# Kernel tuning notes

Measured on AMD Instinct MI355X. Metric: run time of the kernel, lower is better.

## Reference

```python
import jax, jax.numpy as jnp
import numpy as np

N_NODES = 50000
N_EDGES = 800000
IN_DIM, HID_DIM, OUT_DIM = 1024, 256, 512


def setup_inputs() -> dict:
    key = jax.random.key(0)
    ks = jax.random.split(key, 8)
    x = jax.random.normal(ks[0], (N_NODES, IN_DIM), dtype=jnp.float32)
    edge_index = jax.random.randint(ks[1], (2, N_EDGES), 0, N_NODES, dtype=jnp.int64)
    # Glorot-ish scaled weights; PyG SAGEConv: out = lin_l(mean_aggr) + lin_r(x), bias in lin_l
    w1_l = jax.random.normal(ks[2], (HID_DIM, IN_DIM), dtype=jnp.float32) / np.sqrt(IN_DIM)
    w1_r = jax.random.normal(ks[3], (HID_DIM, IN_DIM), dtype=jnp.float32) / np.sqrt(IN_DIM)
    b1 = jnp.zeros((HID_DIM,), dtype=jnp.float32)
    w2_l = jax.random.normal(ks[4], (OUT_DIM, HID_DIM), dtype=jnp.float32) / np.sqrt(HID_DIM)
    w2_r = jax.random.normal(ks[5], (OUT_DIM, HID_DIM), dtype=jnp.float32) / np.sqrt(HID_DIM)
    b2 = jnp.zeros((OUT_DIM,), dtype=jnp.float32)
    return {"x": x, "edge_index": edge_index, "w1_l": w1_l, "w1_r": w1_r, "b1": b1,
            "w2_l": w2_l, "w2_r": w2_r, "b2": b2}


def _sage_conv(x, edge_index, w_l, w_r, b):
    """PyG SAGEConv with mean aggregation: lin_l(mean_{j in N(i)} x_j) + lin_r(x_i)."""
    src, dst = edge_index[0], edge_index[1]
    n = x.shape[0]
    # gather source features and scatter-mean into destinations (the memory-bound part)
    agg = jax.ops.segment_sum(x[src], dst, num_segments=n)          # [N, d_in]
    cnt = jax.ops.segment_sum(jnp.ones_like(src, dtype=x.dtype), dst, num_segments=n)
    mean = agg / jnp.maximum(cnt, 1.0)[:, None]                     # empty neighborhoods -> 0
    return mean @ w_l.T + x @ w_r.T + b


def reference(x, edge_index, w1_l, w1_r, b1, w2_l, w2_r, b2):
    # layer 1 + relu (dropout is identity in eval mode)
    h = jax.nn.relu(_sage_conv(x, edge_index, w1_l, w1_r, b1))
    # final layer, no activation
    return _sage_conv(h, edge_index, w2_l, w2_r, b2)
```

## Files before the change

### kernel.cpp

```cpp
#include <hip/hip_runtime.h>


#define IN_DIM  1024
#define HID_DIM 256
#define OUT_N   512

typedef __attribute__((ext_vector_type(8))) short bf16x8;
typedef __attribute__((ext_vector_type(4))) float f32x4;

static __device__ __forceinline__ unsigned short f2bf(float f) {
  unsigned int u = __float_as_uint(f);
  u += 0x7fffu + ((u >> 16) & 1u);
  return (unsigned short)(u >> 16);
}
static __device__ __forceinline__ float bf2f(unsigned short b) {
  return __uint_as_float(((unsigned int)b) << 16);
}

static __device__ __forceinline__ int load_idx(const void* ei, long long pos, int is64) {
  if (is64) return (int)((const long long*)ei)[pos];
  return ((const int*)ei)[pos];
}

__global__ void k_misc(const unsigned int* __restrict__ ei, int* __restrict__ flag,
                       const float* __restrict__ w1l, const float* __restrict__ w1r,
                       unsigned short* __restrict__ W1c,
                       const float* __restrict__ w2l, const float* __restrict__ w2r,
                       unsigned short* __restrict__ W2c) {
  int b = blockIdx.x;
  if (b == 0) {
    if (threadIdx.x < 64) {
      unsigned int v = ei[2 * threadIdx.x + 1];
      unsigned long long m = __ballot(v == 0u);
      if (threadIdx.x == 0) *flag = (m == ~0ull) ? 1 : 0;
    }
    return;
  }
  b -= 1;
  if (b < 512) {
    int i = b * 256 + threadIdx.x;
    int base = i * 4;
    int n = base / IN_DIM, k = base % IN_DIM;
    const float* s = (n < HID_DIM) ? &w1l[(size_t)n * IN_DIM + k]
                                   : &w1r[(size_t)(n - HID_DIM) * IN_DIM + k];
    float4 v = *(const float4*)s;
    ushort4 o = { f2bf(v.x), f2bf(v.y), f2bf(v.z), f2bf(v.w) };
    *(ushort4*)&W1c[base] = o;
  } else {
    int i = (b - 512) * 256 + threadIdx.x;
    int base = i * 4;
    int n = base >> 9, k = base & 511;
    const float* s = (k < HID_DIM) ? &w2l[(size_t)n * HID_DIM + k]
                                   : &w2r[(size_t)n * HID_DIM + (k - HID_DIM)];
    float4 v = *(const float4*)s;
    ushort4 o = { f2bf(v.x), f2bf(v.y), f2bf(v.z), f2bf(v.w) };
    *(ushort4*)&W2c[base] = o;
  }
}

__global__ void k_cvt_x(const float* __restrict__ x, unsigned short* __restrict__ xbf, int n4) {
  int i = blockIdx.x * 256 + threadIdx.x;
  if (i >= n4) return;
  float4 v = ((const float4*)x)[i];
  ushort4 o = { f2bf(v.x), f2bf(v.y), f2bf(v.z), f2bf(v.w) };
  ((ushort4*)xbf)[i] = o;
}

__global__ void k_deg(const void* ei, int nE, const int* flag, int* deg) {
  int e = blockIdx.x * 256 + threadIdx.x;
  if (e >= nE) return;
  int d = load_idx(ei, (long long)nE + e, *flag);
  atomicAdd(&deg[d], 1);
}

__global__ __launch_bounds__(1024) void k_scan(const int* __restrict__ deg,
                                               int* __restrict__ off, int n) {
  __shared__ int sums[1024];
  int t = threadIdx.x;
  int chunk = (n + 1023) >> 10;
  int base = t * chunk;
  int s = 0;
  for (int i = 0; i < chunk; ++i) { int idx = base + i; if (idx < n) s += deg[idx]; }
  sums[t] = s;
  __syncthreads();
  for (int d = 1; d < 1024; d <<= 1) {
    int v = 0;
    if (t >= d) v = sums[t - d];
    __syncthreads();
    sums[t] += v;
    __syncthreads();
  }
  int run = (t == 0) ? 0 : sums[t - 1];
  for (int i = 0; i < chunk; ++i) {
    int idx = base + i;
    if (idx < n) { off[idx] = run; run += deg[idx]; }
  }
  if (t == 1023) off[n] = run;
}

__global__ void k_fill(const void* ei, int nE, const int* flag,
                       const int* __restrict__ off, int* cursor, int* __restrict__ csr) {
  int e = blockIdx.x * 256 + threadIdx.x;
  if (e >= nE) return;
  int is64 = *flag;
  int s = load_idx(ei, e, is64);
  int d = load_idx(ei, (long long)nE + e, is64);
  int p = atomicAdd(&cursor[d], 1);
  csr[off[d] + p] = s;
}

static __device__ __forceinline__ void load_lds16(const void* g, void* lds) {
  __builtin_amdgcn_global_load_lds(
      (const __attribute__((address_space(1))) unsigned int*)g,
      (__attribute__((address_space(3))) unsigned int*)lds, 16, 0, 0);
}

__global__ __launch_bounds__(256) void k_gemm1(const unsigned short* __restrict__ A,
                                               const unsigned short* __restrict__ B,
                                               unsigned short* __restrict__ Cl,
                                               unsigned short* __restrict__ Cr,
                                               const float* __restrict__ b1) {
  __shared__ unsigned short As[128 * 32];
  __shared__ unsigned short Bs[128 * 32];
  const int tid = threadIdx.x;
  const int w = tid >> 6, l = tid & 63;
  const int wm = w >> 1, wn = w & 1;
  const int quad = l >> 4, lane16 = l & 15;
  const int m0 = blockIdx.y * 128;
  const int n0 = blockIdx.x * 128;

  f32x4 acc[4][4] = {};
  for (int k0 = 0; k0 < IN_DIM; k0 += 32) {
#pragma unroll
    for (int c = 0; c < 2; ++c) {
      const int flat = ((w * 2 + c) << 10);
      const int fb = flat + l * 16;
      const int row = fb >> 6;
      const int cb = fb & 63;
      load_lds16(A + (size_t)(m0 + row) * IN_DIM + (k0 + (cb >> 1)), (char*)As + flat);
      load_lds16(B + (size_t)(n0 + row) * IN_DIM + (k0 + (cb >> 1)), (char*)Bs + flat);
    }
    __syncthreads();
    bf16x8 af[4], bfr[4];
#pragma unroll
    for (int i = 0; i < 4; ++i)
      af[i] = *(const bf16x8*)&As[(wm * 64 + i * 16 + lane16) * 32 + quad * 8];
#pragma unroll
    for (int j = 0; j < 4; ++j)
      bfr[j] = *(const bf16x8*)&Bs[(wn * 64 + j * 16 + lane16) * 32 + quad * 8];
#pragma unroll
    for (int i = 0; i < 4; ++i)
#pragma unroll
      for (int j = 0; j < 4; ++j)
        acc[i][j] = __builtin_amdgcn_mfma_f32_16x16x32_bf16(af[i], bfr[j], acc[i][j], 0, 0, 0);
    __syncthreads();
  }

  const bool right = (n0 >= 256);
  unsigned short* Cb = right ? Cr : Cl;
  const int nc0 = n0 - (right ? 256 : 0);
#pragma unroll
  for (int i = 0; i < 4; ++i) {
    const int rbase = m0 + wm * 64 + i * 16 + quad * 4;
#pragma unroll
    for (int j = 0; j < 4; ++j) {
      const int col = nc0 + wn * 64 + j * 16 + lane16;
      const float bv = right ? b1[col] : 0.0f;
#pragma unroll
      for (int r = 0; r < 4; ++r)
        Cb[(size_t)(rbase + r) * HID_DIM + col] = f2bf(acc[i][j][r] + bv);
    }
  }
}

__global__ __launch_bounds__(256) void k_gemm2(const unsigned short* __restrict__ Am,
                                               const unsigned short* __restrict__ Ah,
                                               const unsigned short* __restrict__ B,
                                               float* __restrict__ out,
                                               const float* __restrict__ b2, int Mstore) {
  __shared__ unsigned short As[128 * 32];
  __shared__ unsigned short Bs[128 * 32];
  const int tid = threadIdx.x;
  const int w = tid >> 6, l = tid & 63;
  const int wm = w >> 1, wn = w & 1;
  const int quad = l >> 4, lane16 = l & 15;
  const int m0 = blockIdx.y * 128;
  const int n0 = blockIdx.x * 128;

  f32x4 acc[4][4] = {};
  for (int k0 = 0; k0 < 2 * HID_DIM; k0 += 32) {
    const unsigned short* Abase = (k0 < HID_DIM) ? Am + k0 : Ah + (k0 - HID_DIM);
#pragma unroll
    for (int c = 0; c < 2; ++c) {
      const int flat = ((w * 2 + c) << 10);
      const int fb = flat + l * 16;
      const int row = fb >> 6;
      const int cb = fb & 63;
      load_lds16(Abase + (size_t)(m0 + row) * HID_DIM + (cb >> 1), (char*)As + flat);
      load_lds16(B + (size_t)(n0 + row) * (2 * HID_DIM) + (k0 + (cb >> 1)), (char*)Bs + flat);
    }
    __syncthreads();
    bf16x8 af[4], bfr[4];
#pragma unroll
    for (int i = 0; i < 4; ++i)
      af[i] = *(const bf16x8*)&As[(wm * 64 + i * 16 + lane16) * 32 + quad * 8];
#pragma unroll
    for (int j = 0; j < 4; ++j)
      bfr[j] = *(const bf16x8*)&Bs[(wn * 64 + j * 16 + lane16) * 32 + quad * 8];
#pragma unroll
    for (int i = 0; i < 4; ++i)
#pragma unroll
      for (int j = 0; j < 4; ++j)
        acc[i][j] = __builtin_amdgcn_mfma_f32_16x16x32_bf16(af[i], bfr[j], acc[i][j], 0, 0, 0);
    __syncthreads();
  }

#pragma unroll
  for (int i = 0; i < 4; ++i) {
    const int rbase = m0 + wm * 64 + i * 16 + quad * 4;
#pragma unroll
    for (int j = 0; j < 4; ++j) {
      const int col = n0 + wn * 64 + j * 16 + lane16;
      const float bv = b2[col];
#pragma unroll
      for (int r = 0; r < 4; ++r) {
        const int rowi = rbase + r;
        if (rowi < Mstore) out[(size_t)rowi * OUT_N + col] = acc[i][j][r] + bv;
      }
    }
  }
}

__global__ void k_agg1(const unsigned short* __restrict__ Cl,
                       const unsigned short* __restrict__ Cr,
                       const int* __restrict__ off, const int* __restrict__ csr,
                       unsigned short* __restrict__ h, int nNodes) {
  int node = blockIdx.x * 4 + (threadIdx.x >> 6);
  int l = threadIdx.x & 63;
  if (node >= nNodes) return;
  int s = off[node], e = off[node + 1];
  float a0 = 0.f, a1 = 0.f, a2 = 0.f, a3 = 0.f;
  int i = s;
  for (; i + 4 <= e; i += 4) {
    int s0 = csr[i], s1 = csr[i + 1], s2 = csr[i + 2], s3 = csr[i + 3];
    ushort4 v0 = *(const ushort4*)&Cl[(size_t)s0 * HID_DIM + l * 4];
    ushort4 v1 = *(const ushort4*)&Cl[(size_t)s1 * HID_DIM + l * 4];
    ushort4 v2 = *(const ushort4*)&Cl[(size_t)s2 * HID_DIM + l * 4];
    ushort4 v3 = *(const ushort4*)&Cl[(size_t)s3 * HID_DIM + l * 4];
    a0 += bf2f(v0.x) + bf2f(v1.x) + bf2f(v2.x) + bf2f(v3.x);
    a1 += bf2f(v0.y) + bf2f(v1.y) + bf2f(v2.y) + bf2f(v3.y);
    a2 += bf2f(v0.z) + bf2f(v1.z) + bf2f(v2.z) + bf2f(v3.z);
    a3 += bf2f(v0.w) + bf2f(v1.w) + bf2f(v2.w) + bf2f(v3.w);
  }
  for (; i < e; ++i) {
    int s0 = csr[i];
    ushort4 v = *(const ushort4*)&Cl[(size_t)s0 * HID_DIM + l * 4];
    a0 += bf2f(v.x); a1 += bf2f(v.y); a2 += bf2f(v.z); a3 += bf2f(v.w);
  }
  float inv = 1.0f / fmaxf((float)(e - s), 1.0f);
  ushort4 xr = *(const ushort4*)&Cr[(size_t)node * HID_DIM + l * 4];
  ushort4 o = { f2bf(fmaxf(a0 * inv + bf2f(xr.x), 0.0f)),
                f2bf(fmaxf(a1 * inv + bf2f(xr.y), 0.0f)),
                f2bf(fmaxf(a2 * inv + bf2f(xr.z), 0.0f)),
                f2bf(fmaxf(a3 * inv + bf2f(xr.w), 0.0f)) };
  *(ushort4*)&h[(size_t)node * HID_DIM + l * 4] = o;
}

__global__ void k_agg2(const unsigned short* __restrict__ h,
                       const int* __restrict__ off, const int* __restrict__ csr,
                       unsigned short* __restrict__ mean2, int nNodes) {
  int node = blockIdx.x * 4 + (threadIdx.x >> 6);
  int l = threadIdx.x & 63;
  if (node >= nNodes) return;
  int s = off[node], e = off[node + 1];
  float a0 = 0.f, a1 = 0.f, a2 = 0.f, a3 = 0.f;
  int i = s;
  for (; i + 4 <= e; i += 4) {
    int s0 = csr[i], s1 = csr[i + 1], s2 = csr[i + 2], s3 = csr[i + 3];
    ushort4 v0 = *(const ushort4*)&h[(size_t)s0 * HID_DIM + l * 4];
    ushort4 v1 = *(const ushort4*)&h[(size_t)s1 * HID_DIM + l * 4];
    ushort4 v2 = *(const ushort4*)&h[(size_t)s2 * HID_DIM + l * 4];
    ushort4 v3 = *(const ushort4*)&h[(size_t)s3 * HID_DIM + l * 4];
    a0 += bf2f(v0.x) + bf2f(v1.x) + bf2f(v2.x) + bf2f(v3.x);
    a1 += bf2f(v0.y) + bf2f(v1.y) + bf2f(v2.y) + bf2f(v3.y);
    a2 += bf2f(v0.z) + bf2f(v1.z) + bf2f(v2.z) + bf2f(v3.z);
    a3 += bf2f(v0.w) + bf2f(v1.w) + bf2f(v2.w) + bf2f(v3.w);
  }
  for (; i < e; ++i) {
    int s0 = csr[i];
    ushort4 v = *(const ushort4*)&h[(size_t)s0 * HID_DIM + l * 4];
    a0 += bf2f(v.x); a1 += bf2f(v.y); a2 += bf2f(v.z); a3 += bf2f(v.w);
  }
  float inv = 1.0f / fmaxf((float)(e - s), 1.0f);
  ushort4 o = { f2bf(a0 * inv), f2bf(a1 * inv), f2bf(a2 * inv), f2bf(a3 * inv) };
  *(ushort4*)&mean2[(size_t)node * HID_DIM + l * 4] = o;
}

extern "C" void kernel_launch(void* const* d_in, const int* in_sizes, int n_in,
                              void* d_out, int out_size, void* d_ws, size_t ws_size,
                              hipStream_t stream) {
  const float* x   = (const float*)d_in[0];
  const void*  ei  = d_in[1];
  const float* w1l = (const float*)d_in[2];
  const float* w1r = (const float*)d_in[3];
  const float* b1  = (const float*)d_in[4];
  const float* w2l = (const float*)d_in[5];
  const float* w2r = (const float*)d_in[6];
  const float* b2  = (const float*)d_in[7];
  float* out = (float*)d_out;

  const int nN   = in_sizes[0] / IN_DIM;
  const int nE   = in_sizes[1] / 2;
  const int Mpad = (nN + 127) & ~127;

  char* ws = (char*)d_ws;
  size_t o = 0;
  auto alloc = [&](size_t bytes) {
    char* p = ws + o;
    o += (bytes + 255) & ~(size_t)255;
    return p;
  };
  unsigned short* xbf   = (unsigned short*)alloc((size_t)Mpad * IN_DIM * 2);
  unsigned short* W1c   = (unsigned short*)alloc((size_t)2 * HID_DIM * IN_DIM * 2);
  unsigned short* W2c   = (unsigned short*)alloc((size_t)OUT_N * 2 * HID_DIM * 2);
  unsigned short* Cl    = (unsigned short*)alloc((size_t)Mpad * HID_DIM * 2);
  unsigned short* Cr    = (unsigned short*)alloc((size_t)Mpad * HID_DIM * 2);
  unsigned short* hbuf  = (unsigned short*)alloc((size_t)Mpad * HID_DIM * 2);
  unsigned short* mean2 = (unsigned short*)alloc((size_t)Mpad * HID_DIM * 2);
  int* deg    = (int*)alloc((size_t)nN * 4);
  int* offs   = (int*)alloc((size_t)(nN + 1) * 4);
  int* cursor = (int*)alloc((size_t)nN * 4);
  int* csr    = (int*)alloc((size_t)nE * 4);
  int* flag   = (int*)alloc(256);

  hipMemsetAsync(deg, 0, (size_t)nN * 4, stream);
  hipMemsetAsync(cursor, 0, (size_t)nN * 4, stream);

  k_misc<<<1 + 512 + 256, 256, 0, stream>>>((const unsigned int*)ei, flag,
                                            w1l, w1r, W1c, w2l, w2r, W2c);
  k_cvt_x<<<(nN * IN_DIM / 4 + 255) / 256, 256, 0, stream>>>(x, xbf, nN * IN_DIM / 4);
  k_deg<<<(nE + 255) / 256, 256, 0, stream>>>(ei, nE, flag, deg);
  k_scan<<<1, 1024, 0, stream>>>(deg, offs, nN);
  k_fill<<<(nE + 255) / 256, 256, 0, stream>>>(ei, nE, flag, offs, cursor, csr);

  dim3 g1(512 / 128, Mpad / 128);
  k_gemm1<<<g1, 256, 0, stream>>>(xbf, W1c, Cl, Cr, b1);
  k_agg1<<<(nN + 3) / 4, 256, 0, stream>>>(Cl, Cr, offs, csr, hbuf, nN);
  k_agg2<<<(nN + 3) / 4, 256, 0, stream>>>(hbuf, offs, csr, mean2, nN);
  k_gemm2<<<g1, 256, 0, stream>>>(mean2, hbuf, W2c, out, b2, nN);
}
```

Baseline: 754.7 us.

## Parallelize degree scan, fuse conversion kernels, XCD-swizzle GEMMs, widen aggregation loads

Replaces the single-block serial scan with a three-kernel block-parallel scan that writes offsets and cursor start positions together, so the fill step stores directly at the cursor value and one memset goes away. It merges the weight and x conversion kernels into one launch and remaps GEMM workgroups across XCDs for better L2 locality. The aggregation kernels now load 16-byte bf16x8 vectors with each half-wave handling alternating neighbours, then combine the halves with a shuffle. The changes add launches and complexity, and the offsets array is no longer sized nN+1, so off[node+1] for the last node relies on the padding entry.

```diff
diff --git a/kernel.cpp b/kernel.cpp
--- a/kernel.cpp
+++ b/kernel.cpp
@@ -22,11 +22,13 @@
   return ((const int*)ei)[pos];
 }
 
-__global__ void k_misc(const unsigned int* __restrict__ ei, int* __restrict__ flag,
-                       const float* __restrict__ w1l, const float* __restrict__ w1r,
-                       unsigned short* __restrict__ W1c,
-                       const float* __restrict__ w2l, const float* __restrict__ w2r,
-                       unsigned short* __restrict__ W2c) {
+__global__ void k_pre(const unsigned int* __restrict__ ei, int* __restrict__ flag,
+                      const float* __restrict__ w1l, const float* __restrict__ w1r,
+                      unsigned short* __restrict__ W1c,
+                      const float* __restrict__ w2l, const float* __restrict__ w2r,
+                      unsigned short* __restrict__ W2c,
+                      const float* __restrict__ x, unsigned short* __restrict__ xbf,
+                      int n4) {
   int b = blockIdx.x;
   if (b == 0) {
     if (threadIdx.x < 64) {
@@ -36,9 +38,8 @@
     }
     return;
   }
-  b -= 1;
-  if (b < 512) {
-    int i = b * 256 + threadIdx.x;
+  if (b < 513) {
+    int i = (b - 1) * 256 + threadIdx.x;
     int base = i * 4;
     int n = base / IN_DIM, k = base % IN_DIM;
     const float* s = (n < HID_DIM) ? &w1l[(size_t)n * IN_DIM + k]
@@ -46,8 +47,10 @@
     float4 v = *(const float4*)s;
     ushort4 o = { f2bf(v.x), f2bf(v.y), f2bf(v.z), f2bf(v.w) };
     *(ushort4*)&W1c[base] = o;
-  } else {
-    int i = (b - 512) * 256 + threadIdx.x;
+    return;
+  }
+  if (b < 769) {
+    int i = (b - 513) * 256 + threadIdx.x;
     int base = i * 4;
     int n = base >> 9, k = base & 511;
     const float* s = (k < HID_DIM) ? &w2l[(size_t)n * HID_DIM + k]
@@ -55,11 +58,9 @@
     float4 v = *(const float4*)s;
     ushort4 o = { f2bf(v.x), f2bf(v.y), f2bf(v.z), f2bf(v.w) };
     *(ushort4*)&W2c[base] = o;
-  }
-}
-
-__global__ void k_cvt_x(const float* __restrict__ x, unsigned short* __restrict__ xbf, int n4) {
-  int i = blockIdx.x * 256 + threadIdx.x;
+    return;
+  }
+  int i = (b - 769) * 256 + threadIdx.x;
   if (i >= n4) return;
   float4 v = ((const float4*)x)[i];
   ushort4 o = { f2bf(v.x), f2bf(v.y), f2bf(v.z), f2bf(v.w) };
@@ -73,46 +74,84 @@
   atomicAdd(&deg[d], 1);
 }
 
-__global__ __launch_bounds__(1024) void k_scan(const int* __restrict__ deg,
-                                               int* __restrict__ off, int n) {
-  __shared__ int sums[1024];
+__global__ void k_bsum(const int* __restrict__ deg, int* __restrict__ bsum) {
   int t = threadIdx.x;
-  int chunk = (n + 1023) >> 10;
-  int base = t * chunk;
-  int s = 0;
-  for (int i = 0; i < chunk; ++i) { int idx = base + i; if (idx < n) s += deg[idx]; }
-  sums[t] = s;
+  int4 d4 = ((const int4*)(deg + (size_t)blockIdx.x * 1024))[t];
+  int v = d4.x + d4.y + d4.z + d4.w;
+#pragma unroll
+  for (int d = 1; d < 64; d <<= 1) v += __shfl_xor(v, d);
+  __shared__ int ws[4];
+  if ((t & 63) == 0) ws[t >> 6] = v;
+  __syncthreads();
+  if (t == 0) bsum[blockIdx.x] = ws[0] + ws[1] + ws[2] + ws[3];
+}
+
+__global__ __launch_bounds__(1024) void k_bscan(int* __restrict__ bsum, int nb) {
+  __shared__ int s[1024];
+  int t = threadIdx.x;
+  s[t] = (t < nb) ? bsum[t] : 0;
   __syncthreads();
   for (int d = 1; d < 1024; d <<= 1) {
-    int v = 0;
-    if (t >= d) v = sums[t - d];
-    __syncthreads();
-    sums[t] += v;
-    __syncthreads();
-  }
-  int run = (t == 0) ? 0 : sums[t - 1];
-  for (int i = 0; i < chunk; ++i) {
-    int idx = base + i;
-    if (idx < n) { off[idx] = run; run += deg[idx]; }
-  }
-  if (t == 1023) off[n] = run;
+    int v = (t >= d) ? s[t - d] : 0;
+    __syncthreads();
+    s[t] += v;
+    __syncthreads();
+  }
+  if (t < nb) bsum[t] = s[t];
+}
+
+__global__ __launch_bounds__(256) void k_offsets(const int* __restrict__ deg,
+                                                 const int* __restrict__ bsumInc,
+                                                 int* __restrict__ off,
+                                                 int* __restrict__ cursor) {
+  const int t = threadIdx.x;
+  const int l = t & 63, w = t >> 6;
+  const size_t base = (size_t)blockIdx.x * 1024;
+  int4 d4 = ((const int4*)(deg + base))[t];
+  int tsum = d4.x + d4.y + d4.z + d4.w;
+  int incl = tsum;
+#pragma unroll
+  for (int d = 1; d < 64; d <<= 1) {
+    int u = __shfl_up(incl, d);
+    if (l >= d) incl += u;
+  }
+  __shared__ int wt[4];
+  if (l == 63) wt[w] = incl;
+  __syncthreads();
+  int wpre = 0;
+  for (int i = 0; i < w; ++i) wpre += wt[i];
+  int bpre = (blockIdx.x == 0) ? 0 : bsumInc[blockIdx.x - 1];
+  int excl = bpre + wpre + incl - tsum;
+  int4 o;
+  o.x = excl;
+  o.y = excl + d4.x;
+  o.z = o.y + d4.y;
+  o.w = o.z + d4.z;
+  ((int4*)(off + base))[t] = o;
+  ((int4*)(cursor + base))[t] = o;
 }
 
 __global__ void k_fill(const void* ei, int nE, const int* flag,
-                       const int* __restrict__ off, int* cursor, int* __restrict__ csr) {
+                       int* cursor, int* __restrict__ csr) {
   int e = blockIdx.x * 256 + threadIdx.x;
   if (e >= nE) return;
   int is64 = *flag;
   int s = load_idx(ei, e, is64);
   int d = load_idx(ei, (long long)nE + e, is64);
   int p = atomicAdd(&cursor[d], 1);
-  csr[off[d] + p] = s;
+  csr[p] = s;
 }
 
 static __device__ __forceinline__ void load_lds16(const void* g, void* lds) {
   __builtin_amdgcn_global_load_lds(
       (const __attribute__((address_space(1))) unsigned int*)g,
       (__attribute__((address_space(3))) unsigned int*)lds, 16, 0, 0);
+}
+
+static __device__ __forceinline__ int xcd_swz(int orig, int nwg) {
+  const int q = nwg >> 3, r = nwg & 7;
+  const int xcd = orig & 7, rk = orig >> 3;
+  return (xcd < r) ? xcd * (q + 1) + rk : r * (q + 1) + (xcd - r) * q + rk;
 }
 
 __global__ __launch_bounds__(256) void k_gemm1(const unsigned short* __restrict__ A,
@@ -126,8 +165,10 @@
   const int w = tid >> 6, l = tid & 63;
   const int wm = w >> 1, wn = w & 1;
   const int quad = l >> 4, lane16 = l & 15;
-  const int m0 = blockIdx.y * 128;
-  const int n0 = blockIdx.x * 128;
+  const int nwg = gridDim.x * gridDim.y;
+  const int wg = xcd_swz(blockIdx.y * gridDim.x + blockIdx.x, nwg);
+  const int m0 = (wg / gridDim.x) * 128;
+  const int n0 = (wg % gridDim.x) * 128;
 
   f32x4 acc[4][4] = {};
   for (int k0 = 0; k0 < IN_DIM; k0 += 32) {
@@ -184,8 +225,10 @@
   const int w = tid >> 6, l = tid & 63;
   const int wm = w >> 1, wn = w & 1;
   const int quad = l >> 4, lane16 = l & 15;
-  const int m0 = blockIdx.y * 128;
-  const int n0 = blockIdx.x * 128;
+  const int nwg = gridDim.x * gridDim.y;
+  const int wg = xcd_swz(blockIdx.y * gridDim.x + blockIdx.x, nwg);
+  const int m0 = (wg / gridDim.x) * 128;
+  const int n0 = (wg % gridDim.x) * 128;
 
   f32x4 acc[4][4] = {};
   for (int k0 = 0; k0 < 2 * HID_DIM; k0 += 32) {
@@ -231,69 +274,107 @@
   }
 }
 
+#define ACC8(v) { a0 += bf2f((unsigned short)(v)[0]); a1 += bf2f((unsigned short)(v)[1]); \
+                  a2 += bf2f((unsigned short)(v)[2]); a3 += bf2f((unsigned short)(v)[3]); \
+                  a4 += bf2f((unsigned short)(v)[4]); a5 += bf2f((unsigned short)(v)[5]); \
+                  a6 += bf2f((unsigned short)(v)[6]); a7 += bf2f((unsigned short)(v)[7]); }
+
 __global__ void k_agg1(const unsigned short* __restrict__ Cl,
                        const unsigned short* __restrict__ Cr,
                        const int* __restrict__ off, const int* __restrict__ csr,
                        unsigned short* __restrict__ h, int nNodes) {
   int node = blockIdx.x * 4 + (threadIdx.x >> 6);
-  int l = threadIdx.x & 63;
   if (node >= nNodes) return;
+  const int l = threadIdx.x & 63;
+  const int half = l >> 5, li = l & 31;
+  const size_t colb = (size_t)li * 8;
   int s = off[node], e = off[node + 1];
-  float a0 = 0.f, a1 = 0.f, a2 = 0.f, a3 = 0.f;
-  int i = s;
-  for (; i + 4 <= e; i += 4) {
-    int s0 = csr[i], s1 = csr[i + 1], s2 = csr[i + 2], s3 = csr[i + 3];
-    ushort4 v0 = *(const ushort4*)&Cl[(size_t)s0 * HID_DIM + l * 4];
-    ushort4 v1 = *(const ushort4*)&Cl[(size_t)s1 * HID_DIM + l * 4];
-    ushort4 v2 = *(const ushort4*)&Cl[(size_t)s2 * HID_DIM + l * 4];
-    ushort4 v3 = *(const ushort4*)&Cl[(size_t)s3 * HID_DIM + l * 4];
-    a0 += bf2f(v0.x) + bf2f(v1.x) + bf2f(v2.x) + bf2f(v3.x);
-    a1 += bf2f(v0.y) + bf2f(v1.y) + bf2f(v2.y) + bf2f(v3.y);
-    a2 += bf2f(v0.z) + bf2f(v1.z) + bf2f(v2.z) + bf2f(v3.z);
-    a3 += bf2f(v0.w) + bf2f(v1.w) + bf2f(v2.w) + bf2f(v3.w);
-  }
-  for (; i < e; ++i) {
-    int s0 = csr[i];
-    ushort4 v = *(const ushort4*)&Cl[(size_t)s0 * HID_DIM + l * 4];
-    a0 += bf2f(v.x); a1 += bf2f(v.y); a2 += bf2f(v.z); a3 += bf2f(v.w);
-  }
-  float inv = 1.0f / fmaxf((float)(e - s), 1.0f);
-  ushort4 xr = *(const ushort4*)&Cr[(size_t)node * HID_DIM + l * 4];
-  ushort4 o = { f2bf(fmaxf(a0 * inv + bf2f(xr.x), 0.0f)),
-                f2bf(fmaxf(a1 * inv + bf2f(xr.y), 0.0f)),
-                f2bf(fmaxf(a2 * inv + bf2f(xr.z), 0.0f)),
-                f2bf(fmaxf(a3 * inv + bf2f(xr.w), 0.0f)) };
-  *(ushort4*)&h[(size_t)node * HID_DIM + l * 4] = o;
-}
-
-__global__ void k_agg2(const unsigned short* __restrict__ h,
+  int cnt = e - s;
+  int P = cnt >> 1;
+  float a0 = 0.f, a1 = 0.f, a2 = 0.f, a3 = 0.f, a4 = 0.f, a5 = 0.f, a6 = 0.f, a7 = 0.f;
+  int k = 0;
+  for (; k + 4 <= P; k += 4) {
+    int ib = s + 2 * k + half;
+    int s0 = csr[ib], s1 = csr[ib + 2], s2 = csr[ib + 4], s3 = csr[ib + 6];
+    bf16x8 v0 = *(const bf16x8*)&Cl[(size_t)s0 * HID_DIM + colb];
+    bf16x8 v1 = *(const bf16x8*)&Cl[(size_t)s1 * HID_DIM + colb];
+    bf16x8 v2 = *(const bf16x8*)&Cl[(size_t)s2 * HID_DIM + colb];
+    bf16x8 v3 = *(const bf16x8*)&Cl[(size_t)s3 * HID_DIM + colb];
+    ACC8(v0); ACC8(v1); ACC8(v2); ACC8(v3);
+  }
+  for (; k < P; ++k) {
+    int ib = s + 2 * k + half;
+    bf16x8 v = *(const bf16x8*)&Cl[(size_t)csr[ib] * HID_DIM + colb];
+    ACC8(v);
+  }
+  if ((cnt & 1) && half == 0) {
+    bf16x8 v = *(const bf16x8*)&Cl[(size_t)csr[e - 1] * HID_DIM + colb];
+    ACC8(v);
+  }
+  a0 += __shfl_xor(a0, 32); a1 += __shfl_xor(a1, 32);
+  a2 += __shfl_xor(a2, 32); a3 += __shfl_xor(a3, 32);
+  a4 += __shfl_xor(a4, 32); a5 += __shfl_xor(a5, 32);
+  a6 += __shfl_xor(a6, 32); a7 += __shfl_xor(a7, 32);
+  if (half == 0) {
+    float inv = 1.0f / fmaxf((float)cnt, 1.0f);
+    bf16x8 xr = *(const bf16x8*)&Cr[(size_t)node * HID_DIM + colb];
+    bf16x8 o;
+    o[0] = (short)f2bf(fmaxf(a0 * inv + bf2f((unsigned short)xr[0]), 0.0f));
+    o[1] = (short)f2bf(fmaxf(a1 * inv + bf2f((unsigned short)xr[1]), 0.0f));
+    o[2] = (short)f2bf(fmaxf(a2 * inv + bf2f((unsigned short)xr[2]), 0.0f));
+    o[3] = (short)f2bf(fmaxf(a3 * inv + bf2f((unsigned short)xr[3]), 0.0f));
+    o[4] = (short)f2bf(fmaxf(a4 * inv + bf2f((unsigned short)xr[4]), 0.0f));
+    o[5] = (short)f2bf(fmaxf(a5 * inv + bf2f((unsigned short)xr[5]), 0.0f));
+    o[6] = (short)f2bf(fmaxf(a6 * inv + bf2f((unsigned short)xr[6]), 0.0f));
+    o[7] = (short)f2bf(fmaxf(a7 * inv + bf2f((unsigned short)xr[7]), 0.0f));
+    *(bf16x8*)&h[(size_t)node * HID_DIM + colb] = o;
+  }
+}
+
+__global__ void k_agg2(const unsigned short* __restrict__ hsrc,
                        const int* __restrict__ off, const int* __restrict__ csr,
                        unsigned short* __restrict__ mean2, int nNodes) {
   int node = blockIdx.x * 4 + (threadIdx.x >> 6);
-  int l = threadIdx.x & 63;
   if (node >= nNodes) return;
+  const int l = threadIdx.x & 63;
+  const int half = l >> 5, li = l & 31;
+  const size_t colb = (size_t)li * 8;
   int s = off[node], e = off[node + 1];
-  float a0 = 0.f, a1 = 0.f, a2 = 0.f, a3 = 0.f;
-  int i = s;
-  for (; i + 4 <= e; i += 4) {
-    int s0 = csr[i], s1 = csr[i + 1], s2 = csr[i + 2], s3 = csr[i + 3];
-    ushort4 v0 = *(const ushort4*)&h[(size_t)s0 * HID_DIM + l * 4];
-    ushort4 v1 = *(const ushort4*)&h[(size_t)s1 * HID_DIM + l * 4];
-    ushort4 v2 = *(const ushort4*)&h[(size_t)s2 * HID_DIM + l * 4];
-    ushort4 v3 = *(const ushort4*)&h[(size_t)s3 * HID_DIM + l * 4];
-    a0 += bf2f(v0.x) + bf2f(v1.x) + bf2f(v2.x) + bf2f(v3.x);
-    a1 += bf2f(v0.y) + bf2f(v1.y) + bf2f(v2.y) + bf2f(v3.y);
-    a2 += bf2f(v0.z) + bf2f(v1.z) + bf2f(v2.z) + bf2f(v3.z);
-    a3 += bf2f(v0.w) + bf2f(v1.w) + bf2f(v2.w) + bf2f(v3.w);
-  }
-  for (; i < e; ++i) {
-    int s0 = csr[i];
-    ushort4 v = *(const ushort4*)&h[(size_t)s0 * HID_DIM + l * 4];
-    a0 += bf2f(v.x); a1 += bf2f(v.y); a2 += bf2f(v.z); a3 += bf2f(v.w);
-  }
-  float inv = 1.0f / fmaxf((float)(e - s), 1.0f);
-  ushort4 o = { f2bf(a0 * inv), f2bf(a1 * inv), f2bf(a2 * inv), f2bf(a3 * inv) };
-  *(ushort4*)&mean2[(size_t)node * HID_DIM + l * 4] = o;
+  int cnt = e - s;
+  int P = cnt >> 1;
+  float a0 = 0.f, a1 = 0.f, a2 = 0.f, a3 = 0.f, a4 = 0.f, a5 = 0.f, a6 = 0.f, a7 = 0.f;
+  int k = 0;
+  for (; k + 4 <= P; k += 4) {
+    int ib = s + 2 * k + half;
+    int s0 = csr[ib], s1 = csr[ib + 2], s2 = csr[ib + 4], s3 = csr[ib + 6];
+    bf16x8 v0 = *(const bf16x8*)&hsrc[(size_t)s0 * HID_DIM + colb];
+    bf16x8 v1 = *(const bf16x8*)&hsrc[(size_t)s1 * HID_DIM + colb];
+    bf16x8 v2 = *(const bf16x8*)&hsrc[(size_t)s2 * HID_DIM + colb];
+    bf16x8 v3 = *(const bf16x8*)&hsrc[(size_t)s3 * HID_DIM + colb];
+    ACC8(v0); ACC8(v1); ACC8(v2); ACC8(v3);
+  }
+  for (; k < P; ++k) {
+    int ib = s + 2 * k + half;
+    bf16x8 v = *(const bf16x8*)&hsrc[(size_t)csr[ib] * HID_DIM + colb];
+    ACC8(v);
+  }
+  if ((cnt & 1) && half == 0) {
+    bf16x8 v = *(const bf16x8*)&hsrc[(size_t)csr[e - 1] * HID_DIM + colb];
+    ACC8(v);
+  }
+  a0 += __shfl_xor(a0, 32); a1 += __shfl_xor(a1, 32);
+  a2 += __shfl_xor(a2, 32); a3 += __shfl_xor(a3, 32);
+  a4 += __shfl_xor(a4, 32); a5 += __shfl_xor(a5, 32);
+  a6 += __shfl_xor(a6, 32); a7 += __shfl_xor(a7, 32);
+  if (half == 0) {
+    float inv = 1.0f / fmaxf((float)cnt, 1.0f);
+    bf16x8 o;
+    o[0] = (short)f2bf(a0 * inv); o[1] = (short)f2bf(a1 * inv);
+    o[2] = (short)f2bf(a2 * inv); o[3] = (short)f2bf(a3 * inv);
+    o[4] = (short)f2bf(a4 * inv); o[5] = (short)f2bf(a5 * inv);
+    o[6] = (short)f2bf(a6 * inv); o[7] = (short)f2bf(a7 * inv);
+    *(bf16x8*)&mean2[(size_t)node * HID_DIM + colb] = o;
+  }
 }
 
 extern "C" void kernel_launch(void* const* d_in, const int* in_sizes, int n_in,
@@ -312,6 +393,8 @@
   const int nN   = in_sizes[0] / IN_DIM;
   const int nE   = in_sizes[1] / 2;
   const int Mpad = (nN + 127) & ~127;
+  const int padN = (nN + 1023) & ~1023;
+  const int nb   = padN >> 10;
 
   char* ws = (char*)d_ws;
   size_t o = 0;
@@ -327,21 +410,24 @@
   unsigned short* Cr    = (unsigned short*)alloc((size_t)Mpad * HID_DIM * 2);
   unsigned short* hbuf  = (unsigned short*)alloc((size_t)Mpad * HID_DIM * 2);
   unsigned short* mean2 = (unsigned short*)alloc((size_t)Mpad * HID_DIM * 2);
-  int* deg    = (int*)alloc((size_t)nN * 4);
-  int* offs   = (int*)alloc((size_t)(nN + 1) * 4);
-  int* cursor = (int*)alloc((size_t)nN * 4);
+  int* deg    = (int*)alloc((size_t)padN * 4);
+  int* offs   = (int*)alloc((size_t)padN * 4);
+  int* cursor = (int*)alloc((size_t)padN * 4);
+  int* bsum   = (int*)alloc((size_t)1024 * 4);
   int* csr    = (int*)alloc((size_t)nE * 4);
   int* flag   = (int*)alloc(256);
 
-  hipMemsetAsync(deg, 0, (size_t)nN * 4, stream);
-  hipMemsetAsync(cursor, 0, (size_t)nN * 4, stream);
-
-  k_misc<<<1 + 512 + 256, 256, 0, stream>>>((const unsigned int*)ei, flag,
-                                            w1l, w1r, W1c, w2l, w2r, W2c);
-  k_cvt_x<<<(nN * IN_DIM / 4 + 255) / 256, 256, 0, stream>>>(x, xbf, nN * IN_DIM / 4);
+  hipMemsetAsync(deg, 0, (size_t)padN * 4, stream);
+
+  const int n4 = nN * IN_DIM / 4;
+  k_pre<<<769 + (n4 + 255) / 256, 256, 0, stream>>>((const unsigned int*)ei, flag,
+                                                    w1l, w1r, W1c, w2l, w2r, W2c,
+                                                    x, xbf, n4);
   k_deg<<<(nE + 255) / 256, 256, 0, stream>>>(ei, nE, flag, deg);
-  k_scan<<<1, 1024, 0, stream>>>(deg, offs, nN);
-  k_fill<<<(nE + 255) / 256, 256, 0, stream>>>(ei, nE, flag, offs, cursor, csr);
+  k_bsum<<<nb, 256, 0, stream>>>(deg, bsum);
+  k_bscan<<<1, 1024, 0, stream>>>(bsum, nb);
+  k_offsets<<<nb, 256, 0, stream>>>(deg, bsum, offs, cursor);
+  k_fill<<<(nE + 255) / 256, 256, 0, stream>>>(ei, nE, flag, cursor, csr);
 
   dim3 g1(512 / 128, Mpad / 128);
   k_gemm1<<<g1, 256, 0, stream>>>(xbf, W1c, Cl, Cr, b1);
```

After: 674.4 us. -10.6%, faster.
